# Kernel optimization log

Hardware: AMD Instinct MI355X
Metric: run time of the kernel (lower is better)

## Reference

```python
import jax, jax.numpy as jnp
import numpy as np

EMBED_DIM = 1024
NUM_HEADS = 16
HEAD_DIM = EMBED_DIM // NUM_HEADS
B, S = 2, 2048
BIG = 1e9  # clamp / nan_to_num saturation value from the torch module


def setup_inputs() -> dict:
    key = jax.random.key(0)
    k1, k2, k3, k4, k5 = jax.random.split(key, 5)
    sc = 1.0 / np.sqrt(EMBED_DIM)
    x = jax.random.normal(k1, (B, S, EMBED_DIM), dtype=jnp.float32)
    qkv_w = jax.random.normal(k2, (3 * EMBED_DIM, EMBED_DIM), dtype=jnp.float32) * sc
    qkv_b = jax.random.normal(k3, (3 * EMBED_DIM,), dtype=jnp.float32) * 0.01
    out_w = jax.random.normal(k4, (EMBED_DIM, EMBED_DIM), dtype=jnp.float32) * sc
    out_b = jax.random.normal(k5, (EMBED_DIM,), dtype=jnp.float32) * 0.01
    # causal mask, broadcastable to [B, H, S, S]; 0 => masked
    mask = jnp.tril(jnp.ones((S, S), dtype=jnp.int32))[None, None, :, :]
    return {"x": x, "mask": mask, "qkv_w": qkv_w, "qkv_b": qkv_b,
            "out_w": out_w, "out_b": out_b}


def reference(x, mask, qkv_w, qkv_b, out_w, out_b):
    b, s, e = x.shape
    # fused QKV projection (torch Linear: x @ W.T + b)
    qkv = x @ qkv_w.T + qkv_b                      # [B, S, 3E]
    q, k, v = jnp.split(qkv, 3, axis=-1)
    def heads(t):
        return t.reshape(b, s, NUM_HEADS, HEAD_DIM).transpose(0, 2, 1, 3)  # [B,H,S,D]
    q, k, v = heads(q), heads(k), heads(v)
    scores = jnp.einsum('bhqd,bhkd->bhqk', q, k) / np.sqrt(HEAD_DIM)
    scores = jnp.clip(scores, -BIG, BIG)
    # masked_fill(mask==0, -inf) then nan_to_num(neginf=-1e9) => masked -> -1e9
    scores = jnp.where(mask == 0, -jnp.inf, scores)
    scores = jnp.nan_to_num(scores, nan=0.0, posinf=BIG, neginf=-BIG)
    scores = scores - jnp.max(scores, axis=-1, keepdims=True)
    attn = jax.nn.softmax(scores, axis=-1) + 1e-9
    out = jnp.einsum('bhqk,bhkd->bhqd', attn, v)   # [B,H,S,D]
    out = out.transpose(0, 2, 1, 3).reshape(b, s, e)
    return out @ out_w.T + out_b
```

## Files before the change

### kernel.cpp

```cpp
#include <hip/hip_runtime.h>
#include <stdint.h>

#define B_ 2
#define H_ 16
#define S_ 2048
#define D_ 64
#define E_ 1024
#define M_ 4096
#define N3_ 3072

typedef __attribute__((ext_vector_type(8))) short bf16x8;
typedef __attribute__((ext_vector_type(4))) float f32x4;
typedef __attribute__((ext_vector_type(16))) float f32x16;
typedef __attribute__((ext_vector_type(4))) unsigned short us4;
typedef __attribute__((ext_vector_type(4))) int i32x4;

__device__ __forceinline__ unsigned short f2b(float f) {
  union { float f; unsigned int u; } v; v.f = f;
  unsigned int r = v.u + 0x7FFFu + ((v.u >> 16) & 1u);
  return (unsigned short)(r >> 16);
}

__device__ __forceinline__ void gll16(const void* g, void* l) {
  __builtin_amdgcn_global_load_lds((const __attribute__((address_space(1))) uint32_t*)g,
                                   (__attribute__((address_space(3))) uint32_t*)l, 16, 0, 0);
}

__global__ __launch_bounds__(256) void f32_to_bf16_k(const float* __restrict__ in,
                                                     unsigned short* __restrict__ out, int n) {
  int i = (blockIdx.x * blockDim.x + threadIdx.x) * 4;
  if (i + 3 < n) {
    float4 v = *(const float4*)(in + i);
    us4 o; o.x = f2b(v.x); o.y = f2b(v.y); o.z = f2b(v.z); o.w = f2b(v.w);
    *(us4*)(out + i) = o;
  }
}

template<int MODE>
__global__ __launch_bounds__(512)
void gemm_bt_k(const unsigned short* __restrict__ A,
               const unsigned short* __restrict__ Bw,
               const float* __restrict__ bias,
               float* __restrict__ outf,
               unsigned short* __restrict__ qo,
               unsigned short* __restrict__ ko,
               unsigned short* __restrict__ vto,
               const int K) {
  __shared__ unsigned short As[2][128 * 32];
  __shared__ unsigned short Bs[2][128 * 32];
  const int tid = threadIdx.x;
  const int wid = tid >> 6, lane = tid & 63;
  const int l4 = lane & 15, lh = lane >> 4;
  const int gx = gridDim.x;
  int id = blockIdx.y * gx + blockIdx.x;
  const int cpx = (gx * gridDim.y) >> 3;
  id = (id & 7) * cpx + (id >> 3);
  const int bm = (id / gx) << 7, bn = (id % gx) << 7;
  const int mq = wid >> 2, nq = wid & 3;
  const int wm = mq << 6, wn = nq << 5;
  f32x4 acc[4][2] = {};
  const int srow = lane >> 2;
  const int scolb = ((lane & 3) ^ (((lane >> 3) & 1) << 1)) << 4;
  auto STAGE = [&](int bb, int kt) {
    const int r = (wid << 4) + srow;
    gll16((const char*)A + ((size_t)(bm + r) * K + kt) * 2 + scolb, &As[bb][wid << 9]);
    gll16((const char*)Bw + ((size_t)(bn + r) * K + kt) * 2 + scolb, &Bs[bb][wid << 9]);
  };
  STAGE(0, 0);
  __syncthreads();
  const int ro = (l4 << 5) + ((lh ^ (((l4 >> 1) & 1) << 1)) << 3);
  for (int kt = 0; kt < K; kt += 32) {
    const int bb = (kt >> 5) & 1;
    if (kt + 32 < K) STAGE(bb ^ 1, kt + 32);
    bf16x8 af[4], bfr[2];
#pragma unroll
    for (int g = 0; g < 4; ++g)
      af[g] = *(const bf16x8*)&As[bb][(((mq << 2) + g) << 9) + ro];
#pragma unroll
    for (int h = 0; h < 2; ++h)
      bfr[h] = *(const bf16x8*)&Bs[bb][(((nq << 1) + h) << 9) + ro];
#pragma unroll
    for (int mg = 0; mg < 4; ++mg)
#pragma unroll
      for (int ng = 0; ng < 2; ++ng)
        acc[mg][ng] = __builtin_amdgcn_mfma_f32_16x16x32_bf16(af[mg], bfr[ng], acc[mg][ng], 0, 0, 0);
    __syncthreads();
  }
#pragma unroll
  for (int mg = 0; mg < 4; ++mg) {
#pragma unroll
    for (int ng = 0; ng < 2; ++ng) {
      const int n = bn + wn + (ng << 4) + l4;
      const float bv = bias[n];
      const int m0 = bm + wm + (mg << 4) + (lh << 2);
      if (MODE == 1) {
#pragma unroll
        for (int i = 0; i < 4; ++i)
          outf[(size_t)(m0 + i) * E_ + n] = acc[mg][ng][i] + bv;
      } else {
        const int region = n >> 10;
        const int nn = n & 1023;
        const int h = nn >> 6, d = nn & 63;
        const int b = m0 >> 11, s0 = m0 & 2047;
        const int bh = (b << 4) + h;
        if (region == 2) {
          us4 pk;
#pragma unroll
          for (int i = 0; i < 4; ++i) pk[i] = f2b(acc[mg][ng][i] + bv);
          *(us4*)&vto[((size_t)bh * D_ + d) * S_ + s0] = pk;
        } else {
          unsigned short* dst = (region == 0) ? qo : ko;
          const float sc = (region == 0) ? 0.125f : 1.0f;
#pragma unroll
          for (int i = 0; i < 4; ++i)
            dst[((size_t)bh * S_ + s0 + i) * D_ + d] = f2b((acc[mg][ng][i] + bv) * sc);
        }
      }
    }
  }
}

__global__ __launch_bounds__(512)
void attn_k(const unsigned short* __restrict__ Q,
            const unsigned short* __restrict__ Kt,
            const unsigned short* __restrict__ Vt,
            unsigned short* __restrict__ O) {
  __shared__ __align__(16) char smem[32768];
  const int tid = threadIdx.x;
  const int wid = tid >> 6, lane = tid & 63;
  const int l31 = lane & 31, hi = lane >> 5, hi4 = hi << 2;
  const int bid = blockIdx.x;
  const int xcd = bid & 7, jj = bid >> 3;
  const int bh = (xcd << 2) + (jj & 3);
  const int pairq = jj >> 2;
  const int qbB = 15 - pairq;
  const int myqb = (wid < 4) ? pairq : qbB;
  const int q0w = (myqb << 7) + ((wid & 3) << 5);
  const int nt = (qbB + 1) << 1;
  const int ntaw = ((q0w + 31) >> 6) + 1;

  const char* Qb = (const char*)Q + (size_t)bh * (S_ * D_ * 2);
  const char* Kb = (const char*)Kt + (size_t)bh * (S_ * D_ * 2);
  const char* Vb = (const char*)Vt + (size_t)bh * (D_ * S_ * 2);

  bf16x8 qf[4];
#pragma unroll
  for (int st = 0; st < 4; ++st)
    qf[st] = *(const bf16x8*)(Qb + (size_t)(q0w + l31) * 128 + (st << 5) + (hi << 4));

  const int sw = wid & 3;
  const int r1 = (sw << 4) + (lane >> 3), r2 = r1 + 8;
  const int cc = lane & 7;
  const int ko1 = (r1 << 7) + ((cc ^ (r1 & 7)) << 4);
  const int ko2 = (r2 << 7) + ((cc ^ (r2 & 7)) << 4);
  const int vo1 = (r1 << 12) + ((cc ^ (r1 & 7)) << 4);
  const int vo2 = (r2 << 12) + ((cc ^ (r2 & 7)) << 4);

  f32x16 oacc[2] = {};
  float m_i = -3.0e38f, l_i = 0.0f;
  const int qg = q0w + l31;
  const int swl = l31 & 7;

  {
    char* kd = smem + (sw << 11);
    char* vd = smem + 16384 + (sw << 11);
    if (wid < 4) { gll16(Kb + ko1, kd); gll16(Kb + ko2, kd + 1024); }
    else         { gll16(Vb + vo1, vd); gll16(Vb + vo2, vd + 1024); }
  }
  __syncthreads();

  for (int t = 0; t < nt; ++t) {
    const int cur = t & 1;
    if (t + 1 < nt) {
      const int nb = cur ^ 1;
      char* kd = smem + (nb << 13) + (sw << 11);
      char* vd = smem + 16384 + (nb << 13) + (sw << 11);
      if (wid < 4) {
        gll16(Kb + (size_t)(t + 1) * 8192 + ko1, kd);
        gll16(Kb + (size_t)(t + 1) * 8192 + ko2, kd + 1024);
      } else {
        gll16(Vb + (size_t)(t + 1) * 128 + vo1, vd);
        gll16(Vb + (size_t)(t + 1) * 128 + vo2, vd + 1024);
      }
    }
    if (t < ntaw) {
      const char* Kc = smem + (cur << 13);
      const char* Vc = smem + 16384 + (cur << 13);
      f32x16 sacc[2] = {};
#pragma unroll
      for (int tt = 0; tt < 2; ++tt)
#pragma unroll
        for (int st = 0; st < 4; ++st) {
          bf16x8 kf = *(const bf16x8*)(Kc + (tt << 12) + (l31 << 7) + ((((st << 1) + hi) ^ swl) << 4));
          sacc[tt] = __builtin_amdgcn_mfma_f32_32x32x16_bf16(kf, qf[st], sacc[tt], 0, 0, 0);
        }
      if (t == ntaw - 1) {
        const int kv0 = t << 6;
#pragma unroll
        for (int tt = 0; tt < 2; ++tt)
#pragma unroll
          for (int r = 0; r < 16; ++r) {
            const int kg = kv0 + (tt << 5) + (r & 3) + ((r >> 2) << 3) + hi4;
            if (kg > qg) sacc[tt][r] = -3.0e38f;
          }
      }
      float pmax = -3.0e38f;
#pragma unroll
      for (int tt = 0; tt < 2; ++tt)
#pragma unroll
        for (int r = 0; r < 16; ++r) pmax = fmaxf(pmax, sacc[tt][r]);
      pmax = fmaxf(pmax, __shfl_xor(pmax, 32));
      if (__any(pmax > m_i + 8.0f)) {
        const float mn = fmaxf(m_i, pmax);
        const float scl = __expf(m_i - mn);
        l_i *= scl;
        m_i = mn;
#pragma unroll
        for (int r = 0; r < 16; ++r) {
          const float sr = __shfl(scl, (r & 3) + ((r >> 2) << 3) + hi4);
          oacc[0][r] *= sr;
          oacc[1][r] *= sr;
        }
      }
#pragma unroll
      for (int tt = 0; tt < 2; ++tt)
#pragma unroll
        for (int r = 0; r < 16; ++r) {
          const float p = __expf(sacc[tt][r] - m_i);
          l_i += p;
          sacc[tt][r] = p;
        }
#pragma unroll
      for (int ks = 0; ks < 4; ++ks) {
        const int tt = ks >> 1, r0 = (ks & 1) << 3;
        int w0, w1, w2, w3;
        asm("v_cvt_pk_bf16_f32 %0, %1, %2" : "=v"(w0) : "v"(sacc[tt][r0 + 0]), "v"(sacc[tt][r0 + 1]));
        asm("v_cvt_pk_bf16_f32 %0, %1, %2" : "=v"(w1) : "v"(sacc[tt][r0 + 2]), "v"(sacc[tt][r0 + 3]));
        asm("v_cvt_pk_bf16_f32 %0, %1, %2" : "=v"(w2) : "v"(sacc[tt][r0 + 4]), "v"(sacc[tt][r0 + 5]));
        asm("v_cvt_pk_bf16_f32 %0, %1, %2" : "=v"(w3) : "v"(sacc[tt][r0 + 6]), "v"(sacc[tt][r0 + 7]));
        asm("v_permlane32_swap_b32 %0, %1" : "+v"(w0), "+v"(w2));
        asm("v_permlane32_swap_b32 %0, %1" : "+v"(w1), "+v"(w3));
        union { i32x4 i; bf16x8 h; } u;
        u.i.x = w0; u.i.y = w1; u.i.z = w2; u.i.w = w3;
        const bf16x8 pa = u.h;
#pragma unroll
        for (int dt = 0; dt < 2; ++dt) {
          bf16x8 vf = *(const bf16x8*)(Vc + (dt << 12) + (l31 << 7) + ((((ks << 1) + hi) ^ swl) << 4));
          oacc[dt] = __builtin_amdgcn_mfma_f32_32x32x16_bf16(pa, vf, oacc[dt], 0, 0, 0);
        }
      }
    }
    __syncthreads();
  }

  const float ltot = l_i + __shfl_xor(l_i, 32);
  const float inv = 1.0f / ltot;
  const int b = bh >> 4, h = bh & 15;
#pragma unroll
  for (int r = 0; r < 16; ++r) {
    const int qr = (r & 3) + ((r >> 2) << 3) + hi4;
    const float ivr = __shfl(inv, qr);
    const size_t off = ((size_t)((b << 11) + q0w + qr) << 10) + (h << 6) + l31;
    O[off]      = f2b(oacc[0][r] * ivr);
    O[off + 32] = f2b(oacc[1][r] * ivr);
  }
}

extern "C" void kernel_launch(void* const* d_in, const int* in_sizes, int n_in,
                              void* d_out, int out_size, void* d_ws, size_t ws_size,
                              hipStream_t stream) {
  const float* x     = (const float*)d_in[0];
  const float* qkv_w = (const float*)d_in[2];
  const float* qkv_b = (const float*)d_in[3];
  const float* out_w = (const float*)d_in[4];
  const float* out_b = (const float*)d_in[5];

  unsigned short* ws   = (unsigned short*)d_ws;
  unsigned short* xb   = ws;
  unsigned short* wqkv = xb + (size_t)M_ * E_;
  unsigned short* wout = wqkv + (size_t)N3_ * E_;
  unsigned short* qB   = wout + (size_t)E_ * E_;
  unsigned short* kB   = qB + (size_t)32 * S_ * D_;
  unsigned short* vtB  = kB + (size_t)32 * S_ * D_;
  unsigned short* oB   = ws;

  f32_to_bf16_k<<<(M_ * E_) / 1024, 256, 0, stream>>>(x, xb, M_ * E_);
  f32_to_bf16_k<<<(N3_ * E_) / 1024, 256, 0, stream>>>(qkv_w, wqkv, N3_ * E_);
  f32_to_bf16_k<<<(E_ * E_) / 1024, 256, 0, stream>>>(out_w, wout, E_ * E_);

  gemm_bt_k<0><<<dim3(N3_ / 128, M_ / 128), 512, 0, stream>>>(
      xb, wqkv, qkv_b, nullptr, qB, kB, vtB, E_);

  attn_k<<<256, 512, 0, stream>>>(qB, kB, vtB, oB);

  gemm_bt_k<1><<<dim3(E_ / 128, M_ / 128), 512, 0, stream>>>(
      oB, wout, out_b, (float*)d_out, nullptr, nullptr, nullptr, E_);
}
```

Before: 110.4 us.

## Split paired causal q-block workgroups into separate 4-wave blocks

Each attention workgroup previously held 8 waves covering two mirrored q-blocks (pairq and 15-pairq) that shared K/V tiles, with the early-finishing half idling. Now each 256-thread block handles one 128-row q-block, and the block order issues the heavy blocks first (15..8), then the light ones (0..7). Every wave loads both K and V. This is meant to remove the intra-block imbalance and raise occupancy, at the cost of loading the K/V stream separately for each block instead of sharing it.

```diff
diff --git a/kernel.cpp b/kernel.cpp
--- a/kernel.cpp
+++ b/kernel.cpp
@@ -120,7 +120,7 @@
   }
 }
 
-__global__ __launch_bounds__(512)
+__global__ __launch_bounds__(256)
 void attn_k(const unsigned short* __restrict__ Q,
             const unsigned short* __restrict__ Kt,
             const unsigned short* __restrict__ Vt,
@@ -130,13 +130,12 @@
   const int wid = tid >> 6, lane = tid & 63;
   const int l31 = lane & 31, hi = lane >> 5, hi4 = hi << 2;
   const int bid = blockIdx.x;
-  const int xcd = bid & 7, jj = bid >> 3;
-  const int bh = (xcd << 2) + (jj & 3);
-  const int pairq = jj >> 2;
-  const int qbB = 15 - pairq;
-  const int myqb = (wid < 4) ? pairq : qbB;
-  const int q0w = (myqb << 7) + ((wid & 3) << 5);
-  const int nt = (qbB + 1) << 1;
+  const int xcd = bid & 7, ii = bid >> 3;
+  const int bh = (xcd << 2) + (ii & 3);
+  const int j = ii >> 2;
+  const int qb = (j < 8) ? (15 - j) : (j - 8);
+  const int q0w = (qb << 7) + (wid << 5);
+  const int nt = (qb + 1) << 1;
   const int ntaw = ((q0w + 31) >> 6) + 1;
 
   const char* Qb = (const char*)Q + (size_t)bh * (S_ * D_ * 2);
@@ -148,8 +147,7 @@
   for (int st = 0; st < 4; ++st)
     qf[st] = *(const bf16x8*)(Qb + (size_t)(q0w + l31) * 128 + (st << 5) + (hi << 4));
 
-  const int sw = wid & 3;
-  const int r1 = (sw << 4) + (lane >> 3), r2 = r1 + 8;
+  const int r1 = (wid << 4) + (lane >> 3), r2 = r1 + 8;
   const int cc = lane & 7;
   const int ko1 = (r1 << 7) + ((cc ^ (r1 & 7)) << 4);
   const int ko2 = (r2 << 7) + ((cc ^ (r2 & 7)) << 4);
@@ -162,10 +160,10 @@
   const int swl = l31 & 7;
 
   {
-    char* kd = smem + (sw << 11);
-    char* vd = smem + 16384 + (sw << 11);
-    if (wid < 4) { gll16(Kb + ko1, kd); gll16(Kb + ko2, kd + 1024); }
-    else         { gll16(Vb + vo1, vd); gll16(Vb + vo2, vd + 1024); }
+    char* kd = smem + (wid << 11);
+    char* vd = smem + 16384 + (wid << 11);
+    gll16(Kb + ko1, kd); gll16(Kb + ko2, kd + 1024);
+    gll16(Vb + vo1, vd); gll16(Vb + vo2, vd + 1024);
   }
   __syncthreads();
 
@@ -173,15 +171,12 @@
     const int cur = t & 1;
     if (t + 1 < nt) {
       const int nb = cur ^ 1;
-      char* kd = smem + (nb << 13) + (sw << 11);
-      char* vd = smem + 16384 + (nb << 13) + (sw << 11);
-      if (wid < 4) {
-        gll16(Kb + (size_t)(t + 1) * 8192 + ko1, kd);
-        gll16(Kb + (size_t)(t + 1) * 8192 + ko2, kd + 1024);
-      } else {
-        gll16(Vb + (size_t)(t + 1) * 128 + vo1, vd);
-        gll16(Vb + (size_t)(t + 1) * 128 + vo2, vd + 1024);
-      }
+      char* kd = smem + (nb << 13) + (wid << 11);
+      char* vd = smem + 16384 + (nb << 13) + (wid << 11);
+      gll16(Kb + (size_t)(t + 1) * 8192 + ko1, kd);
+      gll16(Kb + (size_t)(t + 1) * 8192 + ko2, kd + 1024);
+      gll16(Vb + (size_t)(t + 1) * 128 + vo1, vd);
+      gll16(Vb + (size_t)(t + 1) * 128 + vo2, vd + 1024);
     }
     if (t < ntaw) {
       const char* Kc = smem + (cur << 13);
@@ -291,7 +286,7 @@
   gemm_bt_k<0><<<dim3(N3_ / 128, M_ / 128), 512, 0, stream>>>(
       xb, wqkv, qkv_b, nullptr, qB, kB, vtB, E_);
 
-  attn_k<<<256, 512, 0, stream>>>(qB, kB, vtB, oB);
+  attn_k<<<512, 256, 0, stream>>>(qB, kB, vtB, oB);
 
   gemm_bt_k<1><<<dim3(E_ / 128, M_ / 128), 512, 0, stream>>>(
       oB, wout, out_b, (float*)d_out, nullptr, nullptr, nullptr, E_);
```

New measurement: 116.8 us. 1.06x slower.
